# Kernel tuning notes

Measured on AMD Instinct MI355X. Metric: run time of the kernel, lower is better.

The kernel has to match this reference:

```python
import jax, jax.numpy as jnp
import numpy as np


def setup_inputs() -> dict:
    key = jax.random.key(0)
    ks = jax.random.split(key, 4)
    B, C, H, W = 4, 512, 64, 64
    A = 512  # attention_dim
    x = jax.random.normal(ks[0], (B, C, H, W), dtype=jnp.float32)
    # 1x1 conv weights as [out_ch, in_ch] matrices (kaiming-like scale)
    scale = np.sqrt(2.0 / C).astype(np.float32)
    Wq = jax.random.normal(ks[1], (A, C), dtype=jnp.float32) * scale
    Wk = jax.random.normal(ks[2], (A, C), dtype=jnp.float32) * scale
    Wv = jax.random.normal(ks[3], (C, C), dtype=jnp.float32) * scale
    bq = jnp.zeros((A,), dtype=jnp.float32)
    bk = jnp.zeros((A,), dtype=jnp.float32)
    bv = jnp.zeros((C,), dtype=jnp.float32)
    return {"x": x, "Wq": Wq, "bq": bq, "Wk": Wk, "bk": bk, "Wv": Wv, "bv": bv}


def reference(x, Wq, bq, Wk, bk, Wv, bv):
    B, C, H, W = x.shape
    N = H * W
    xf = x.reshape(B, C, N)  # [B, C, N]
    # 1x1 convs == per-pixel channel matmuls
    q = jnp.einsum('ac,bcn->bna', Wq, xf) + bq[None, None, :]   # [B, N, A] (query, permuted)
    k = jnp.einsum('ac,bcn->ban', Wk, xf) + bk[None, :, None]   # [B, A, N] (key)
    v = jnp.einsum('oc,bcn->bno', Wv, xf) + bv[None, None, :]   # [B, N, C] (value, permuted)
    attn = jnp.einsum('bna,bam->bnm', q, k)                     # [B, N, N]
    attn = jax.nn.softmax(attn, axis=-2)                        # softmax over dim=-2 (queries)
    out = jnp.einsum('bnm,bmc->bnc', attn, v)                   # [B, N, C]
    # Faithful to torch: .view(B, C, H, W) reinterprets the [B, N, C] buffer
    out = out.reshape(B, C, H, W)
    return x + 0.1 * out
```

## Files before the change

### kernel.cpp

```cpp
#include <hip/hip_runtime.h>
#include <stdint.h>


#define LDT 40

typedef _Float16 f16x8 __attribute__((ext_vector_type(8)));
typedef float f32x4 __attribute__((ext_vector_type(4)));

template <int ASRC, int EPI>
__global__ void __launch_bounds__(256, 2) gemm_f16(
    const void* __restrict__ Ap, long lda, long zsa,
    const _Float16* __restrict__ Bp, long ldb, long zsb,
    int kslice,
    const float* __restrict__ lse, long zsl,
    float* __restrict__ outF, _Float16* __restrict__ outH, long ldc, long zso,
    const float* __restrict__ bias0, const float* __restrict__ bias1,
    const float* __restrict__ xadd,
    float* __restrict__ pmax, float* __restrict__ psum, long zsp,
    float alpha)
{
  __shared__ _Float16 sA[128 * LDT];
  __shared__ _Float16 sB[128 * LDT];

  const int z = blockIdx.z;
  const long i0 = (long)blockIdx.x * 128;
  const long j0 = (long)blockIdx.y * 128;
  const int t = (int)threadIdx.x;
  const int lane = t & 63;
  const int wv = t >> 6;
  const int quad = lane >> 4;
  const int lrow = lane & 15;
  const int wm = (wv & 1) << 6;
  const int wn = (wv >> 1) << 6;
  const int r0 = t >> 2;
  const int s0 = (t & 3) << 3;

  const _Float16* gB0 = Bp + z * zsb + (j0 + r0) * ldb + s0;
  const _Float16* gB1 = gB0 + 64 * ldb;
  const int la0 = r0 * LDT + s0;
  const int la1 = (r0 + 64) * LDT + s0;

  const _Float16* gA0 = nullptr;
  const _Float16* gA1 = nullptr;
  const float* fsZ = nullptr;
  gA0 = (const _Float16*)Ap + z * zsa + (i0 + r0) * lda + s0;
  gA1 = gA0 + 64 * lda;
  if constexpr (ASRC == 1) {
    fsZ = lse + z * zsl + (long)blockIdx.x * 4096 + s0;
  }

  f32x4 acc[4][4];
  const f32x4 fz = {0.f, 0.f, 0.f, 0.f};
#pragma unroll
  for (int a = 0; a < 4; a++)
#pragma unroll
    for (int b = 0; b < 4; b++) acc[a][b] = fz;

  for (int kk = 0; kk < kslice; kk += 32) {
    f16x8 a0 = *(const f16x8*)(gA0 + kk);
    f16x8 a1 = *(const f16x8*)(gA1 + kk);
    f16x8 b0 = *(const f16x8*)(gB0 + kk);
    f16x8 b1 = *(const f16x8*)(gB1 + kk);
    if constexpr (ASRC == 1) {
      float4 f0 = *(const float4*)(fsZ + kk);
      float4 f1 = *(const float4*)(fsZ + kk + 4);
      f16x8 fv;
      fv[0] = (_Float16)f0.x; fv[1] = (_Float16)f0.y;
      fv[2] = (_Float16)f0.z; fv[3] = (_Float16)f0.w;
      fv[4] = (_Float16)f1.x; fv[5] = (_Float16)f1.y;
      fv[6] = (_Float16)f1.z; fv[7] = (_Float16)f1.w;
      a0 = a0 * fv;
      a1 = a1 * fv;
    }
    __syncthreads();
    *(f16x8*)&sA[la0] = a0;
    *(f16x8*)&sA[la1] = a1;
    *(f16x8*)&sB[la0] = b0;
    *(f16x8*)&sB[la1] = b1;
    __syncthreads();

    f16x8 fa[4], fb[4];
#pragma unroll
    for (int f = 0; f < 4; f++) {
      fa[f] = *(const f16x8*)&sA[(wm + f * 16 + lrow) * LDT + quad * 8];
      fb[f] = *(const f16x8*)&sB[(wn + f * 16 + lrow) * LDT + quad * 8];
    }
#pragma unroll
    for (int fm = 0; fm < 4; fm++)
#pragma unroll
      for (int fn = 0; fn < 4; fn++)
        acc[fm][fn] = __builtin_amdgcn_mfma_f32_16x16x32_f16(fa[fm], fb[fn], acc[fm][fn], 0, 0, 0);
  }

  const long obase = (long)z * zso;

  if constexpr (EPI == 1 || EPI == 2) {
#pragma unroll
    for (int fm = 0; fm < 4; fm++) {
      const long gi0 = i0 + wm + fm * 16 + quad * 4;
#pragma unroll
      for (int fn = 0; fn < 4; fn++) {
        const long gj = j0 + wn + fn * 16 + lrow;
        float badd = 0.f;
        if constexpr (EPI == 1) badd = (gj < 512) ? bias0[gj] : bias1[gj - 512];
#pragma unroll
        for (int r = 0; r < 4; r++) {
          float v = acc[fm][fn][r];
          if constexpr (EPI == 1) v += badd;
          else v += bias0[gi0 + r];
          outH[obase + (gi0 + r) * ldc + gj] = (_Float16)v;
        }
      }
    }
  } else if constexpr (EPI == 3) {
#pragma unroll
    for (int fm = 0; fm < 4; fm++) {
      const long gi0 = i0 + wm + fm * 16 + quad * 4;
#pragma unroll
      for (int fn = 0; fn < 4; fn++) {
        const long gj = j0 + wn + fn * 16 + lrow;
#pragma unroll
        for (int r = 0; r < 4; r++) {
          const long o = obase + (gi0 + r) * ldc + gj;
          outF[o] = fmaf(alpha, acc[fm][fn][r], xadd[o]);
        }
      }
    }
  } else {
    __syncthreads();
    float* Ls = (float*)sA;
#pragma unroll
    for (int fn = 0; fn < 4; fn++) {
      float mx = -3.4e38f;
#pragma unroll
      for (int fm = 0; fm < 4; fm++)
#pragma unroll
        for (int r = 0; r < 4; r++) mx = fmaxf(mx, acc[fm][fn][r]);
      float sm = 0.f;
#pragma unroll
      for (int fm = 0; fm < 4; fm++)
#pragma unroll
        for (int r = 0; r < 4; r++) sm += __expf(acc[fm][fn][r] - mx);
      Ls[(wv * 4 + quad) * 64 + fn * 16 + lrow] = mx;
      Ls[1024 + (wv * 4 + quad) * 64 + fn * 16 + lrow] = sm;
    }
    __syncthreads();
    {
      const int c = t & 127;
      const int h = t >> 7;
      const int wvv = ((c >> 6) << 1) + h;
      const int wc = c & 63;
      float M = -3.4e38f, Ss = 0.f;
#pragma unroll
      for (int q = 0; q < 4; q++) {
        float m2 = Ls[(wvv * 4 + q) * 64 + wc];
        float s2 = Ls[1024 + (wvv * 4 + q) * 64 + wc];
        float nm = fmaxf(M, m2);
        Ss = Ss * __expf(M - nm) + s2 * __expf(m2 - nm);
        M = nm;
      }
      Ls[2048 + h * 128 + c] = M;
      Ls[2304 + h * 128 + c] = Ss;
    }
    __syncthreads();
    if (t < 128) {
      float m0 = Ls[2048 + t], m1 = Ls[2048 + 128 + t];
      float sa = Ls[2304 + t], sb = Ls[2304 + 128 + t];
      float nm = fmaxf(m0, m1);
      float s = sa * __expf(m0 - nm) + sb * __expf(m1 - nm);
      const long pidx = z * zsp + (long)blockIdx.x * 4096 + j0 + t;
      pmax[pidx] = nm;
      psum[pidx] = s;
      Ls[t] = nm;
    }
    __syncthreads();
#pragma unroll
    for (int fn = 0; fn < 4; fn++) {
      const int colc = wn + fn * 16 + lrow;
      const float Mcol = Ls[colc];
      const long gj = j0 + colc;
#pragma unroll
      for (int fm = 0; fm < 4; fm++) {
        const long gi0 = i0 + wm + fm * 16 + quad * 4;
#pragma unroll
        for (int r = 0; r < 4; r++)
          outH[obase + (gi0 + r) * ldc + gj] = (_Float16)__expf(acc[fm][fn][r] - Mcol);
      }
    }
  }
}

__global__ void convert_weights(const float* __restrict__ Wq, const float* __restrict__ Wk,
                                const float* __restrict__ Wv,
                                _Float16* __restrict__ WQK, _Float16* __restrict__ Wv16)
{
  int idx = blockIdx.x * 256 + threadIdx.x;
  if (idx < 524288)
    WQK[idx] = (_Float16)((idx < 262144) ? Wq[idx] : Wk[idx - 262144]);
  else
    Wv16[idx - 524288] = (_Float16)Wv[idx - 524288];
}

__global__ void transpose_x(const float* __restrict__ x, _Float16* __restrict__ xT)
{
  __shared__ float tile[32][33];
  const int b = blockIdx.z;
  const int n0 = blockIdx.x * 32;
  const int c0 = blockIdx.y * 32;
  const int tx = threadIdx.x;
  const int ty = threadIdx.y;
  const float* xb = x + (long)b * 2097152;
#pragma unroll
  for (int k = 0; k < 4; k++)
    tile[ty + k * 8][tx] = xb[(long)(c0 + ty + k * 8) * 4096 + n0 + tx];
  __syncthreads();
  _Float16* xTb = xT + (long)b * 2097152;
#pragma unroll
  for (int k = 0; k < 4; k++)
    xTb[(long)(n0 + ty + k * 8) * 512 + c0 + tx] = (_Float16)tile[tx][ty + k * 8];
}

__global__ void stats_final(const float* __restrict__ pmax, const float* __restrict__ psum,
                            float* __restrict__ lse)
{
  const int idx = blockIdx.x * 256 + threadIdx.x;
  const int z = idx >> 12;
  const int m = idx & 4095;
  const float* pm = pmax + (long)z * 131072 + m;
  const float* ps = psum + (long)z * 131072 + m;
  float M = -3.4e38f, S = 0.f;
  for (int i = 0; i < 32; i++) {
    float m2 = pm[(long)i * 4096], s2 = ps[(long)i * 4096];
    float nm = fmaxf(M, m2);
    S = S * __expf(M - nm) + s2 * __expf(m2 - nm);
    M = nm;
  }
  lse[idx] = M + __logf(S);
}

__global__ void scale_factors(const float* __restrict__ pmax, const float* __restrict__ lse,
                              float* __restrict__ fscale)
{
  const int idx = blockIdx.x * 256 + threadIdx.x;
  const int z = idx >> 17;
  const int m = idx & 4095;
  fscale[idx] = __expf(pmax[idx] - lse[(z << 12) + m]);
}

extern "C" void kernel_launch(void* const* d_in, const int* in_sizes, int n_in,
                              void* d_out, int out_size, void* d_ws, size_t ws_size,
                              hipStream_t stream)
{
  const float* x  = (const float*)d_in[0];
  const float* Wq = (const float*)d_in[1];
  const float* bq = (const float*)d_in[2];
  const float* Wk = (const float*)d_in[3];
  const float* bk = (const float*)d_in[4];
  const float* Wv = (const float*)d_in[5];
  const float* bv = (const float*)d_in[6];
  float* out = (float*)d_out;

  char* w = (char*)d_ws;
  _Float16* WQK   = (_Float16*)(w + 0);
  _Float16* Wv16  = (_Float16*)(w + 1048576);
  _Float16* xT    = (_Float16*)(w + 1572864);
  _Float16* QK    = (_Float16*)(w + 18350080);
  _Float16* Vt    = (_Float16*)(w + 51904512);
  float*    lse   = (float*)   (w + 68681728);
  float*    pmaxB = (float*)   (w + 68747264);
  float*    psumB = (float*)   (w + 70844416);
  float*    fscal = (float*)   (w + 72941568);
  _Float16* S16   = (_Float16*)(w + 75038720);

  convert_weights<<<3072, 256, 0, stream>>>(Wq, Wk, Wv, WQK, Wv16);
  transpose_x<<<dim3(128, 16, 4), dim3(32, 8), 0, stream>>>(x, xT);

  gemm_f16<0, 1><<<dim3(32, 8, 4), 256, 0, stream>>>(
      xT, 512, 2097152L, WQK, 512, 0L, 512, nullptr, 0L,
      nullptr, QK, 1024, 4194304L, bq, bk, nullptr, nullptr, nullptr, 0L, 0.f);
  gemm_f16<0, 2><<<dim3(4, 32, 4), 256, 0, stream>>>(
      Wv16, 512, 0L, xT, 512, 2097152L, 512, nullptr, 0L,
      nullptr, Vt, 4096, 2097152L, bv, nullptr, nullptr, nullptr, nullptr, 0L, 0.f);
  gemm_f16<0, 4><<<dim3(32, 32, 4), 256, 0, stream>>>(
      QK, 1024, 4194304L, QK + 512, 1024, 4194304L, 512, nullptr, 0L,
      nullptr, S16, 4096, 16777216L, nullptr, nullptr, nullptr,
      pmaxB, psumB, 131072L, 0.f);
  stats_final<<<64, 256, 0, stream>>>(pmaxB, psumB, lse);
  scale_factors<<<2048, 256, 0, stream>>>(pmaxB, lse, fscal);
  gemm_f16<1, 3><<<dim3(32, 4, 4), 256, 0, stream>>>(
      S16, 4096, 16777216L, Vt, 4096, 2097152L, 4096, fscal, 131072L,
      out, nullptr, 512, 2097152L, nullptr, nullptr, x, nullptr, nullptr, 0L, 0.1f);
}
```

Measured before the change: 367.9 us.

## Load GEMM tiles directly into LDS via global_load_lds and use fp16 scale factors

Replaces the register-staged global-to-LDS copy in the f16 GEMM with direct global_load_lds DMA instructions into an unpadded 32-wide LDS layout. The softmax scale factors are stored as fp16, and the scaling is applied to the A fragments after they are read from LDS rather than before staging. This cuts VGPR traffic, load-store instructions and scale-factor bandwidth. In exchange, dropping the padding may cause LDS bank conflicts on fragment reads, and the loop keeps a single buffer behind two barriers with no prefetch overlap. An unused f2bf helper is also added.

After: 381.4 us. 1.04x slower.

```diff
diff --git a/kernel.cpp b/kernel.cpp
--- a/kernel.cpp
+++ b/kernel.cpp
@@ -2,25 +2,36 @@
 #include <stdint.h>
 
 
-#define LDT 40
-
 typedef _Float16 f16x8 __attribute__((ext_vector_type(8)));
 typedef float f32x4 __attribute__((ext_vector_type(4)));
 
+__device__ __forceinline__ void dma16(const void* g, void* l) {
+  __builtin_amdgcn_global_load_lds(
+      (const __attribute__((address_space(1))) uint32_t*)(uintptr_t)g,
+      (__attribute__((address_space(3))) uint32_t*)(uint32_t)(uintptr_t)l, 16, 0, 0);
+}
+
+__device__ __forceinline__ uint16_t f2bf(float f) {
+  uint32_t u = __float_as_uint(f);
+  u += 0x7FFFu + ((u >> 16) & 1u);
+  return (uint16_t)(u >> 16);
+}
+
 template <int ASRC, int EPI>
 __global__ void __launch_bounds__(256, 2) gemm_f16(
-    const void* __restrict__ Ap, long lda, long zsa,
+    const _Float16* __restrict__ Ap, long lda, long zsa,
     const _Float16* __restrict__ Bp, long ldb, long zsb,
     int kslice,
-    const float* __restrict__ lse, long zsl,
+    const _Float16* __restrict__ fs16, long zsl,
     float* __restrict__ outF, _Float16* __restrict__ outH, long ldc, long zso,
     const float* __restrict__ bias0, const float* __restrict__ bias1,
     const float* __restrict__ xadd,
     float* __restrict__ pmax, float* __restrict__ psum, long zsp,
     float alpha)
 {
-  __shared__ _Float16 sA[128 * LDT];
-  __shared__ _Float16 sB[128 * LDT];
+  __shared__ _Float16 smem[8192];
+  _Float16* sA = smem;
+  _Float16* sB = smem + 4096;
 
   const int z = blockIdx.z;
   const long i0 = (long)blockIdx.x * 128;
@@ -32,22 +43,22 @@
   const int lrow = lane & 15;
   const int wm = (wv & 1) << 6;
   const int wn = (wv >> 1) << 6;
-  const int r0 = t >> 2;
-  const int s0 = (t & 3) << 3;
-
-  const _Float16* gB0 = Bp + z * zsb + (j0 + r0) * ldb + s0;
-  const _Float16* gB1 = gB0 + 64 * ldb;
-  const int la0 = r0 * LDT + s0;
-  const int la1 = (r0 + 64) * LDT + s0;
-
-  const _Float16* gA0 = nullptr;
-  const _Float16* gA1 = nullptr;
-  const float* fsZ = nullptr;
-  gA0 = (const _Float16*)Ap + z * zsa + (i0 + r0) * lda + s0;
-  gA1 = gA0 + 64 * lda;
-  if constexpr (ASRC == 1) {
-    fsZ = lse + z * zsl + (long)blockIdx.x * 4096 + s0;
-  }
+
+  const int idx0 = wv * 2;
+  const int srow = lane >> 2;
+  const int sseg = (lane & 3) << 3;
+  const _Float16* gA0 = Ap + z * zsa + (i0 + idx0 * 16 + srow) * lda + sseg;
+  const _Float16* gA1 = gA0 + 16 * lda;
+  const _Float16* gB0 = Bp + z * zsb + (j0 + idx0 * 16 + srow) * ldb + sseg;
+  const _Float16* gB1 = gB0 + 16 * ldb;
+  _Float16* lA0 = sA + idx0 * 512;
+  _Float16* lA1 = lA0 + 512;
+  _Float16* lB0 = sB + idx0 * 512;
+  _Float16* lB1 = lB0 + 512;
+
+  const _Float16* fsZ = nullptr;
+  if constexpr (ASRC == 1)
+    fsZ = fs16 + z * zsl + (long)blockIdx.x * 4096 + quad * 8;
 
   f32x4 acc[4][4];
   const f32x4 fz = {0.f, 0.f, 0.f, 0.f};
@@ -57,33 +68,23 @@
     for (int b = 0; b < 4; b++) acc[a][b] = fz;
 
   for (int kk = 0; kk < kslice; kk += 32) {
-    f16x8 a0 = *(const f16x8*)(gA0 + kk);
-    f16x8 a1 = *(const f16x8*)(gA1 + kk);
-    f16x8 b0 = *(const f16x8*)(gB0 + kk);
-    f16x8 b1 = *(const f16x8*)(gB1 + kk);
+    __syncthreads();
+    dma16(gA0 + kk, lA0);
+    dma16(gA1 + kk, lA1);
+    dma16(gB0 + kk, lB0);
+    dma16(gB1 + kk, lB1);
+    __syncthreads();
+
+    f16x8 fa[4], fb[4];
+#pragma unroll
+    for (int f = 0; f < 4; f++) {
+      fa[f] = *(const f16x8*)&sA[(wm + f * 16 + lrow) * 32 + quad * 8];
+      fb[f] = *(const f16x8*)&sB[(wn + f * 16 + lrow) * 32 + quad * 8];
+    }
     if constexpr (ASRC == 1) {
-      float4 f0 = *(const float4*)(fsZ + kk);
-      float4 f1 = *(const float4*)(fsZ + kk + 4);
-      f16x8 fv;
-      fv[0] = (_Float16)f0.x; fv[1] = (_Float16)f0.y;
-      fv[2] = (_Float16)f0.z; fv[3] = (_Float16)f0.w;
-      fv[4] = (_Float16)f1.x; fv[5] = (_Float16)f1.y;
-      fv[6] = (_Float16)f1.z; fv[7] = (_Float16)f1.w;
-      a0 = a0 * fv;
-      a1 = a1 * fv;
-    }
-    __syncthreads();
-    *(f16x8*)&sA[la0] = a0;
-    *(f16x8*)&sA[la1] = a1;
-    *(f16x8*)&sB[la0] = b0;
-    *(f16x8*)&sB[la1] = b1;
-    __syncthreads();
-
-    f16x8 fa[4], fb[4];
-#pragma unroll
-    for (int f = 0; f < 4; f++) {
-      fa[f] = *(const f16x8*)&sA[(wm + f * 16 + lrow) * LDT + quad * 8];
-      fb[f] = *(const f16x8*)&sB[(wn + f * 16 + lrow) * LDT + quad * 8];
+      const f16x8 fsv = *(const f16x8*)(fsZ + kk);
+#pragma unroll
+      for (int f = 0; f < 4; f++) fa[f] = fa[f] * fsv;
     }
 #pragma unroll
     for (int fm = 0; fm < 4; fm++)
@@ -128,7 +129,7 @@
     }
   } else {
     __syncthreads();
-    float* Ls = (float*)sA;
+    float* Ls = (float*)smem;
 #pragma unroll
     for (int fn = 0; fn < 4; fn++) {
       float mx = -3.4e38f;
@@ -239,12 +240,12 @@
 }
 
 __global__ void scale_factors(const float* __restrict__ pmax, const float* __restrict__ lse,
-                              float* __restrict__ fscale)
+                              _Float16* __restrict__ fs16)
 {
   const int idx = blockIdx.x * 256 + threadIdx.x;
   const int z = idx >> 17;
   const int m = idx & 4095;
-  fscale[idx] = __expf(pmax[idx] - lse[(z << 12) + m]);
+  fs16[idx] = (_Float16)__expf(pmax[idx] - lse[(z << 12) + m]);
 }
 
 extern "C" void kernel_launch(void* const* d_in, const int* in_sizes, int n_in,
@@ -269,7 +270,7 @@
   float*    lse   = (float*)   (w + 68681728);
   float*    pmaxB = (float*)   (w + 68747264);
   float*    psumB = (float*)   (w + 70844416);
-  float*    fscal = (float*)   (w + 72941568);
+  _Float16* fs16  = (_Float16*)(w + 72941568);
   _Float16* S16   = (_Float16*)(w + 75038720);
 
   convert_weights<<<3072, 256, 0, stream>>>(Wq, Wk, Wv, WQK, Wv16);
@@ -286,8 +287,8 @@
       nullptr, S16, 4096, 16777216L, nullptr, nullptr, nullptr,
       pmaxB, psumB, 131072L, 0.f);
   stats_final<<<64, 256, 0, stream>>>(pmaxB, psumB, lse);
-  scale_factors<<<2048, 256, 0, stream>>>(pmaxB, lse, fscal);
+  scale_factors<<<2048, 256, 0, stream>>>(pmaxB, lse, fs16);
   gemm_f16<1, 3><<<dim3(32, 4, 4), 256, 0, stream>>>(
-      S16, 4096, 16777216L, Vt, 4096, 2097152L, 4096, fscal, 131072L,
+      S16, 4096, 16777216L, Vt, 4096, 2097152L, 4096, fs16, 131072L,
       out, nullptr, 512, 2097152L, nullptr, nullptr, x, nullptr, nullptr, 0L, 0.1f);
 }
```
